# Kernel tuning notes

Measured on AMD Instinct MI355X. Metric: run time of the kernel, lower is better.

## Reference

```python
import jax, jax.numpy as jnp
import numpy as np


def setup_inputs() -> dict:
    key = jax.random.key(0)
    x = jax.random.normal(key, (16384, 4096), dtype=jnp.float32)
    return {"x": x, "k": 64}


def reference(x, k):
    # allow_negative_topk=False -> select and output based on ReLU(x)
    scores = jax.nn.relu(x)                      # [N, D]
    kk = min(k, scores.shape[-1])
    _, topk_idx = jax.lax.top_k(scores, kk)      # [N, kk]
    rows = jnp.arange(scores.shape[0])[:, None]  # [N, 1]
    mask = jnp.zeros_like(scores).at[rows, topk_idx].set(1.0)
    return scores * mask
```

## Files before the change

### kernel.cpp

```cpp
#include <hip/hip_runtime.h>


constexpr int ROW_LEN = 4096;
constexpr int TPB     = 256;
constexpr int SEG     = 128;
constexpr unsigned int KPRE_BITS = 0x3FC00000u;

typedef float f32x4 __attribute__((ext_vector_type(4)));

__global__ __launch_bounds__(TPB, 4)
void topk_relu_kernel(const float* __restrict__ x, const int* __restrict__ kptr,
                      float* __restrict__ out, int rows)
{
    __shared__ alignas(16) int hist[256];
    __shared__ unsigned int cand[4 * SEG];
    __shared__ int scnt[4];
    __shared__ unsigned int selT;
    __shared__ int selNeed;
    __shared__ int wtot[4];
    __shared__ unsigned long long wtot64[4];
    __shared__ int sel_digit, sel_kk, sel_flag;

    const int row = blockIdx.x;
    if (row >= rows) return;
    const int tid  = threadIdx.x;
    const int lane = tid & 63;
    const int wid  = tid >> 6;

    int k = *kptr;
    if (k > ROW_LEN) k = ROW_LEN;

    const float* __restrict__ xrow = x + (size_t)row * ROW_LEN;
    unsigned int key[16];
#pragma unroll
    for (int j = 0; j < 4; ++j) {
        f32x4 v = *(const f32x4*)(xrow + j * 1024 + tid * 4);
#pragma unroll
        for (int c = 0; c < 4; ++c)
            key[4 * j + c] = __float_as_uint(fmaxf(v[c], 0.0f));
    }

    int base = 0;
#pragma unroll
    for (int j = 0; j < 16; ++j) {
        const bool p = key[j] > KPRE_BITS;
        const unsigned long long mask = __ballot(p);
        const int prior = __builtin_amdgcn_mbcnt_hi(
            (unsigned int)(mask >> 32),
            __builtin_amdgcn_mbcnt_lo((unsigned int)mask, 0));
        const int idx = base + prior;
        if (p && idx < SEG) cand[(wid << 7) + idx] = key[j];
        base += (int)__popcll(mask);
    }
    if (lane == 0) scnt[wid] = base;
    __syncthreads();

    const int c0 = scnt[0], c1 = scnt[1], c2 = scnt[2], c3 = scnt[3];
    const int cnt = c0 + c1 + c2 + c3;
    const bool segok = (c0 <= SEG) & (c1 <= SEG) & (c2 <= SEG) & (c3 <= SEG);

    unsigned int T;
    int need;

    if (cnt >= k && segok) {
        if (wid == 0) {
            const int sc[4] = {c0, c1, c2, c3};
            unsigned int c[8];
#pragma unroll
            for (int i = 0; i < 8; ++i) {
                const int s   = i >> 1;
                const int off = lane + 64 * (i & 1);
                c[i] = (off < sc[s]) ? cand[(s << 7) + off] : 0u;
            }
            int kk = k;
            unsigned int prefix = 0;
#pragma unroll
            for (int p = 0; p < 4; ++p) {
                const int shift = 24 - 8 * p;
                ((int4*)hist)[lane] = make_int4(0, 0, 0, 0);
#pragma unroll
                for (int i = 0; i < 8; ++i) {
                    const unsigned int ci = c[i];
                    if (ci != 0u && (p == 0 || (ci >> (shift + 8)) == prefix))
                        atomicAdd(&hist[(ci >> shift) & 255u], 1);
                }
                const int4 h = ((const int4*)hist)[lane];
                const int h0 = h.x, h1 = h.y, h2 = h.z, h3 = h.w;
                const int lsum = h0 + h1 + h2 + h3;
                int suf = lsum;
#pragma unroll
                for (int d = 1; d < 64; d <<= 1) {
                    int v = __shfl_down(suf, d);
                    if (lane < 64 - d) suf += v;
                }
                const unsigned long long mm = __ballot(suf >= kk);
                const int L = 63 - __clzll(mm);
                int dig = 0, kkn = 0;
                if (lane == L) {
                    int cum = suf - lsum;
                    const int hh[4] = {h0, h1, h2, h3};
#pragma unroll
                    for (int b = 3; b >= 0; --b) {
                        if (cum + hh[b] >= kk) { dig = lane * 4 + b; kkn = kk - cum; break; }
                        cum += hh[b];
                    }
                }
                dig = __shfl(dig, L);
                kk  = __shfl(kkn, L);
                prefix = (prefix << 8) | (unsigned int)dig;
            }
            if (lane == 0) { selT = prefix; selNeed = kk; }
        }

        __syncthreads();
        T = selT;
        need = selNeed;
    } else {
        int kk = k;
        unsigned int prefix = 0;
        int t0 = 0;
        for (int p = 0; p < 4; ++p) {
            const int shift = 24 - 8 * p;
            hist[tid & 255] = 0;
            if (tid == 0) sel_flag = 0;
            __syncthreads();
#pragma unroll
            for (int j = 0; j < 16; ++j) {
                const unsigned int kj = key[j];
                if (kj != 0u && (p == 0 || (kj >> (shift + 8)) == prefix))
                    atomicAdd(&hist[(kj >> shift) & 255u], 1);
            }
            __syncthreads();
            if (tid < 64) {
                const int b0 = tid * 4;
                const int h0 = hist[b0 + 0], h1 = hist[b0 + 1];
                const int h2 = hist[b0 + 2], h3 = hist[b0 + 3];
                const int lsum = h0 + h1 + h2 + h3;
                int suf = lsum;
#pragma unroll
                for (int d = 1; d < 64; d <<= 1) {
                    int v = __shfl_down(suf, d);
                    if (lane < 64 - d) suf += v;
                }
                const unsigned long long mm = __ballot(suf >= kk);
                if (mm == 0ull) {
                    if (lane == 0) sel_flag = 1;
                } else {
                    const int L = 63 - __clzll(mm);
                    if (lane == L) {
                        int cum = suf - lsum;
                        const int hh[4] = {h0, h1, h2, h3};
#pragma unroll
                        for (int b = 3; b >= 0; --b) {
                            if (cum + hh[b] >= kk) { sel_digit = b0 + b; sel_kk = kk - cum; break; }
                            cum += hh[b];
                        }
                    }
                }
            }
            __syncthreads();
            if (sel_flag) { t0 = 1; break; }
            prefix = (prefix << 8) | (unsigned int)sel_digit;
            kk = sel_kk;
            __syncthreads();
        }
        if (t0) { T = 0u; need = 0; }
        else    { T = prefix; need = kk; }
    }

    int eqc = 0;
#pragma unroll
    for (int j = 0; j < 16; ++j) eqc += (key[j] == T) ? 1 : 0;
    int wsum = eqc;
#pragma unroll
    for (int d = 1; d < 64; d <<= 1) wsum += __shfl_down(wsum, d);
    if (lane == 0) wtot[wid] = wsum;
    __syncthreads();
    const int tot = wtot[0] + wtot[1] + wtot[2] + wtot[3];

    float* __restrict__ orow = out + (size_t)row * ROW_LEN;

    if (tot == need) {
#pragma unroll
        for (int j = 0; j < 4; ++j) {
            f32x4 v;
#pragma unroll
            for (int c2 = 0; c2 < 4; ++c2) {
                const unsigned int kj = key[4 * j + c2];
                v[c2] = (kj >= T && T != 0u) ? __uint_as_float(kj) : 0.0f;
            }
            *(f32x4*)(orow + j * 1024 + tid * 4) = v;
        }
    } else {
        unsigned long long packed = 0ull;
#pragma unroll
        for (int j = 0; j < 4; ++j) {
            int e = 0;
#pragma unroll
            for (int c = 0; c < 4; ++c) e += (key[4 * j + c] == T) ? 1 : 0;
            packed |= (unsigned long long)e << (16 * j);
        }
        unsigned long long incp = packed;
#pragma unroll
        for (int d = 1; d < 64; d <<= 1) {
            unsigned long long v = __shfl_up(incp, d);
            if (lane >= d) incp += v;
        }
        if (lane == 63) wtot64[wid] = incp;
        __syncthreads();
        unsigned long long b64 = 0ull;
        for (int w = 0; w < wid; ++w) b64 += wtot64[w];
        const unsigned long long exclp = b64 + incp - packed;
        const unsigned long long t64 = wtot64[0] + wtot64[1] + wtot64[2] + wtot64[3];
        int S[4];
        S[0] = 0;
        S[1] = (int)(t64 & 0xFFFFull);
        S[2] = S[1] + (int)((t64 >> 16) & 0xFFFFull);
        S[3] = S[2] + (int)((t64 >> 32) & 0xFFFFull);
#pragma unroll
        for (int j = 0; j < 4; ++j) {
            int rr = S[j] + (int)((exclp >> (16 * j)) & 0xFFFFull);
            f32x4 v;
#pragma unroll
            for (int c2 = 0; c2 < 4; ++c2) {
                const unsigned int kj = key[4 * j + c2];
                const bool eq = (kj == T);
                const bool keep = (kj > T) || (eq && rr < need);
                v[c2] = keep ? __uint_as_float(kj) : 0.0f;
                rr += eq ? 1 : 0;
            }
            *(f32x4*)(orow + j * 1024 + tid * 4) = v;
        }
    }
}

extern "C" void kernel_launch(void* const* d_in, const int* in_sizes, int n_in,
                              void* d_out, int out_size, void* d_ws, size_t ws_size,
                              hipStream_t stream)
{
    const float* x    = (const float*)d_in[0];
    const int*   kptr = (const int*)d_in[1];
    float*       out  = (float*)d_out;
    const int rows = in_sizes[0] / ROW_LEN;
    topk_relu_kernel<<<rows, TPB, 0, stream>>>(x, kptr, out, rows);
}
```

Baseline: 100.1 us.

## Process one row per wavefront instead of one row per block

```diff
diff --git a/kernel.cpp b/kernel.cpp
--- a/kernel.cpp
+++ b/kernel.cpp
@@ -3,7 +3,7 @@
 
 constexpr int ROW_LEN = 4096;
 constexpr int TPB     = 256;
-constexpr int SEG     = 128;
+constexpr int CAP     = 512;
 constexpr unsigned int KPRE_BITS = 0x3FC00000u;
 
 typedef float f32x4 __attribute__((ext_vector_type(4)));
@@ -12,88 +12,120 @@
 void topk_relu_kernel(const float* __restrict__ x, const int* __restrict__ kptr,
                       float* __restrict__ out, int rows)
 {
-    __shared__ alignas(16) int hist[256];
-    __shared__ unsigned int cand[4 * SEG];
-    __shared__ int scnt[4];
-    __shared__ unsigned int selT;
-    __shared__ int selNeed;
-    __shared__ int wtot[4];
-    __shared__ unsigned long long wtot64[4];
-    __shared__ int sel_digit, sel_kk, sel_flag;
-
-    const int row = blockIdx.x;
-    if (row >= rows) return;
+    __shared__ unsigned int cand4[4][CAP];
+    __shared__ alignas(16) int hist4[4][256];
+
     const int tid  = threadIdx.x;
     const int lane = tid & 63;
     const int wid  = tid >> 6;
 
+    const int row = blockIdx.x * 4 + wid;
+    if (row >= rows) return;
+
     int k = *kptr;
     if (k > ROW_LEN) k = ROW_LEN;
 
     const float* __restrict__ xrow = x + (size_t)row * ROW_LEN;
-    unsigned int key[16];
-#pragma unroll
-    for (int j = 0; j < 4; ++j) {
-        f32x4 v = *(const f32x4*)(xrow + j * 1024 + tid * 4);
+    unsigned int key[64];
+#pragma unroll
+    for (int j = 0; j < 16; ++j) {
+        f32x4 v = *(const f32x4*)(xrow + j * 256 + lane * 4);
 #pragma unroll
         for (int c = 0; c < 4; ++c)
             key[4 * j + c] = __float_as_uint(fmaxf(v[c], 0.0f));
     }
 
-    int base = 0;
-#pragma unroll
-    for (int j = 0; j < 16; ++j) {
+    unsigned int* __restrict__ cand = &cand4[wid][0];
+    int* __restrict__ hist = &hist4[wid][0];
+
+    int cnt = 0;
+#pragma unroll
+    for (int j = 0; j < 64; ++j) {
         const bool p = key[j] > KPRE_BITS;
         const unsigned long long mask = __ballot(p);
         const int prior = __builtin_amdgcn_mbcnt_hi(
             (unsigned int)(mask >> 32),
             __builtin_amdgcn_mbcnt_lo((unsigned int)mask, 0));
-        const int idx = base + prior;
-        if (p && idx < SEG) cand[(wid << 7) + idx] = key[j];
-        base += (int)__popcll(mask);
-    }
-    if (lane == 0) scnt[wid] = base;
-    __syncthreads();
-
-    const int c0 = scnt[0], c1 = scnt[1], c2 = scnt[2], c3 = scnt[3];
-    const int cnt = c0 + c1 + c2 + c3;
-    const bool segok = (c0 <= SEG) & (c1 <= SEG) & (c2 <= SEG) & (c3 <= SEG);
+        const int idx = cnt + prior;
+        if (p && idx < CAP) cand[idx] = key[j];
+        cnt += (int)__popcll(mask);
+    }
 
     unsigned int T;
     int need;
 
-    if (cnt >= k && segok) {
-        if (wid == 0) {
-            const int sc[4] = {c0, c1, c2, c3};
-            unsigned int c[8];
+    if (cnt >= k && cnt <= CAP) {
+        unsigned int c[8];
+#pragma unroll
+        for (int i = 0; i < 8; ++i) {
+            const int off = lane + 64 * i;
+            c[i] = (off < cnt) ? cand[off] : 0u;
+        }
+        int kk = k;
+        unsigned int prefix = 0;
+#pragma unroll
+        for (int p = 0; p < 4; ++p) {
+            const int shift = 24 - 8 * p;
+            ((int4*)hist)[lane] = make_int4(0, 0, 0, 0);
 #pragma unroll
             for (int i = 0; i < 8; ++i) {
-                const int s   = i >> 1;
-                const int off = lane + 64 * (i & 1);
-                c[i] = (off < sc[s]) ? cand[(s << 7) + off] : 0u;
-            }
-            int kk = k;
-            unsigned int prefix = 0;
-#pragma unroll
-            for (int p = 0; p < 4; ++p) {
-                const int shift = 24 - 8 * p;
-                ((int4*)hist)[lane] = make_int4(0, 0, 0, 0);
-#pragma unroll
-                for (int i = 0; i < 8; ++i) {
-                    const unsigned int ci = c[i];
-                    if (ci != 0u && (p == 0 || (ci >> (shift + 8)) == prefix))
-                        atomicAdd(&hist[(ci >> shift) & 255u], 1);
+                const unsigned int ci = c[i];
+                if (ci != 0u && (p == 0 || (ci >> (shift + 8)) == prefix))
+                    atomicAdd(&hist[(ci >> shift) & 255u], 1);
+            }
+            const int4 h = ((const int4*)hist)[lane];
+            const int h0 = h.x, h1 = h.y, h2 = h.z, h3 = h.w;
+            const int lsum = h0 + h1 + h2 + h3;
+            int suf = lsum;
+#pragma unroll
+            for (int d = 1; d < 64; d <<= 1) {
+                int v = __shfl_down(suf, d);
+                if (lane < 64 - d) suf += v;
+            }
+            const unsigned long long mm = __ballot(suf >= kk);
+            const int L = 63 - __clzll(mm);
+            int dig = 0, kkn = 0;
+            if (lane == L) {
+                int cum = suf - lsum;
+                const int hh[4] = {h0, h1, h2, h3};
+#pragma unroll
+                for (int b = 3; b >= 0; --b) {
+                    if (cum + hh[b] >= kk) { dig = lane * 4 + b; kkn = kk - cum; break; }
+                    cum += hh[b];
                 }
-                const int4 h = ((const int4*)hist)[lane];
-                const int h0 = h.x, h1 = h.y, h2 = h.z, h3 = h.w;
-                const int lsum = h0 + h1 + h2 + h3;
-                int suf = lsum;
-#pragma unroll
-                for (int d = 1; d < 64; d <<= 1) {
-                    int v = __shfl_down(suf, d);
-                    if (lane < 64 - d) suf += v;
-                }
-                const unsigned long long mm = __ballot(suf >= kk);
+            }
+            dig = __shfl(dig, L);
+            kk  = __shfl(kkn, L);
+            prefix = (prefix << 8) | (unsigned int)dig;
+        }
+        T = prefix;
+        need = kk;
+    } else {
+        int kk = k;
+        unsigned int prefix = 0;
+        bool t0 = false;
+        for (int p = 0; p < 4 && !t0; ++p) {
+            const int shift = 24 - 8 * p;
+            ((int4*)hist)[lane] = make_int4(0, 0, 0, 0);
+#pragma unroll
+            for (int j = 0; j < 64; ++j) {
+                const unsigned int kj = key[j];
+                if (kj != 0u && (p == 0 || (kj >> (shift + 8)) == prefix))
+                    atomicAdd(&hist[(kj >> shift) & 255u], 1);
+            }
+            const int4 h = ((const int4*)hist)[lane];
+            const int h0 = h.x, h1 = h.y, h2 = h.z, h3 = h.w;
+            const int lsum = h0 + h1 + h2 + h3;
+            int suf = lsum;
+#pragma unroll
+            for (int d = 1; d < 64; d <<= 1) {
+                int v = __shfl_down(suf, d);
+                if (lane < 64 - d) suf += v;
+            }
+            const unsigned long long mm = __ballot(suf >= kk);
+            if (mm == 0ull) {
+                t0 = true;
+            } else {
                 const int L = 63 - __clzll(mm);
                 int dig = 0, kkn = 0;
                 if (lane == L) {
@@ -109,60 +141,6 @@
                 kk  = __shfl(kkn, L);
                 prefix = (prefix << 8) | (unsigned int)dig;
             }
-            if (lane == 0) { selT = prefix; selNeed = kk; }
-        }
-
-        __syncthreads();
-        T = selT;
-        need = selNeed;
-    } else {
-        int kk = k;
-        unsigned int prefix = 0;
-        int t0 = 0;
-        for (int p = 0; p < 4; ++p) {
-            const int shift = 24 - 8 * p;
-            hist[tid & 255] = 0;
-            if (tid == 0) sel_flag = 0;
-            __syncthreads();
-#pragma unroll
-            for (int j = 0; j < 16; ++j) {
-                const unsigned int kj = key[j];
-                if (kj != 0u && (p == 0 || (kj >> (shift + 8)) == prefix))
-                    atomicAdd(&hist[(kj >> shift) & 255u], 1);
-            }
-            __syncthreads();
-            if (tid < 64) {
-                const int b0 = tid * 4;
-                const int h0 = hist[b0 + 0], h1 = hist[b0 + 1];
-                const int h2 = hist[b0 + 2], h3 = hist[b0 + 3];
-                const int lsum = h0 + h1 + h2 + h3;
-                int suf = lsum;
-#pragma unroll
-                for (int d = 1; d < 64; d <<= 1) {
-                    int v = __shfl_down(suf, d);
-                    if (lane < 64 - d) suf += v;
-                }
-                const unsigned long long mm = __ballot(suf >= kk);
-                if (mm == 0ull) {
-                    if (lane == 0) sel_flag = 1;
-                } else {
-                    const int L = 63 - __clzll(mm);
-                    if (lane == L) {
-                        int cum = suf - lsum;
-                        const int hh[4] = {h0, h1, h2, h3};
-#pragma unroll
-                        for (int b = 3; b >= 0; --b) {
-                            if (cum + hh[b] >= kk) { sel_digit = b0 + b; sel_kk = kk - cum; break; }
-                            cum += hh[b];
-                        }
-                    }
-                }
-            }
-            __syncthreads();
-            if (sel_flag) { t0 = 1; break; }
-            prefix = (prefix << 8) | (unsigned int)sel_digit;
-            kk = sel_kk;
-            __syncthreads();
         }
         if (t0) { T = 0u; need = 0; }
         else    { T = prefix; need = kk; }
@@ -170,56 +148,59 @@
 
     int eqc = 0;
 #pragma unroll
-    for (int j = 0; j < 16; ++j) eqc += (key[j] == T) ? 1 : 0;
-    int wsum = eqc;
-#pragma unroll
-    for (int d = 1; d < 64; d <<= 1) wsum += __shfl_down(wsum, d);
-    if (lane == 0) wtot[wid] = wsum;
-    __syncthreads();
-    const int tot = wtot[0] + wtot[1] + wtot[2] + wtot[3];
+    for (int j = 0; j < 64; ++j) eqc += (key[j] == T) ? 1 : 0;
+    int tot = eqc;
+#pragma unroll
+    for (int d = 1; d < 64; d <<= 1) tot += __shfl_xor(tot, d);
 
     float* __restrict__ orow = out + (size_t)row * ROW_LEN;
 
     if (tot == need) {
 #pragma unroll
-        for (int j = 0; j < 4; ++j) {
+        for (int j = 0; j < 16; ++j) {
             f32x4 v;
 #pragma unroll
             for (int c2 = 0; c2 < 4; ++c2) {
                 const unsigned int kj = key[4 * j + c2];
                 v[c2] = (kj >= T && T != 0u) ? __uint_as_float(kj) : 0.0f;
             }
-            *(f32x4*)(orow + j * 1024 + tid * 4) = v;
+            *(f32x4*)(orow + j * 256 + lane * 4) = v;
         }
     } else {
-        unsigned long long packed = 0ull;
-#pragma unroll
-        for (int j = 0; j < 4; ++j) {
-            int e = 0;
-#pragma unroll
-            for (int c = 0; c < 4; ++c) e += (key[4 * j + c] == T) ? 1 : 0;
-            packed |= (unsigned long long)e << (16 * j);
-        }
-        unsigned long long incp = packed;
-#pragma unroll
-        for (int d = 1; d < 64; d <<= 1) {
-            unsigned long long v = __shfl_up(incp, d);
-            if (lane >= d) incp += v;
-        }
-        if (lane == 63) wtot64[wid] = incp;
-        __syncthreads();
-        unsigned long long b64 = 0ull;
-        for (int w = 0; w < wid; ++w) b64 += wtot64[w];
-        const unsigned long long exclp = b64 + incp - packed;
-        const unsigned long long t64 = wtot64[0] + wtot64[1] + wtot64[2] + wtot64[3];
-        int S[4];
+        unsigned long long exclp[4];
+        int totj[16];
+#pragma unroll
+        for (int q = 0; q < 4; ++q) {
+            unsigned long long pk = 0ull;
+#pragma unroll
+            for (int jj = 0; jj < 4; ++jj) {
+                const int j = 4 * q + jj;
+                int e = 0;
+#pragma unroll
+                for (int c = 0; c < 4; ++c) e += (key[4 * j + c] == T) ? 1 : 0;
+                pk |= (unsigned long long)e << (16 * jj);
+            }
+            unsigned long long incp = pk;
+#pragma unroll
+            for (int d = 1; d < 64; d <<= 1) {
+                unsigned long long v = __shfl_up(incp, d);
+                if (lane >= d) incp += v;
+            }
+            exclp[q] = incp - pk;
+            const unsigned long long t = __shfl(incp, 63);
+#pragma unroll
+            for (int jj = 0; jj < 4; ++jj)
+                totj[4 * q + jj] = (int)((t >> (16 * jj)) & 0xFFFFull);
+        }
+        int S[16];
         S[0] = 0;
-        S[1] = (int)(t64 & 0xFFFFull);
-        S[2] = S[1] + (int)((t64 >> 16) & 0xFFFFull);
-        S[3] = S[2] + (int)((t64 >> 32) & 0xFFFFull);
-#pragma unroll
-        for (int j = 0; j < 4; ++j) {
-            int rr = S[j] + (int)((exclp >> (16 * j)) & 0xFFFFull);
+#pragma unroll
+        for (int j = 1; j < 16; ++j) S[j] = S[j - 1] + totj[j - 1];
+
+#pragma unroll
+        for (int j = 0; j < 16; ++j) {
+            const int q = j >> 2, jj = j & 3;
+            int rr = S[j] + (int)((exclp[q] >> (16 * jj)) & 0xFFFFull);
             f32x4 v;
 #pragma unroll
             for (int c2 = 0; c2 < 4; ++c2) {
@@ -229,7 +210,7 @@
                 v[c2] = keep ? __uint_as_float(kj) : 0.0f;
                 rr += eq ? 1 : 0;
             }
-            *(f32x4*)(orow + j * 1024 + tid * 4) = v;
+            *(f32x4*)(orow + j * 256 + lane * 4) = v;
         }
     }
 }
@@ -242,5 +223,6 @@
     const int*   kptr = (const int*)d_in[1];
     float*       out  = (float*)d_out;
     const int rows = in_sizes[0] / ROW_LEN;
-    topk_relu_kernel<<<rows, TPB, 0, stream>>>(x, kptr, out, rows);
+    const int nb = (rows + 3) / 4;
+    topk_relu_kernel<<<nb, TPB, 0, stream>>>(x, kptr, out, rows);
 }
```

Result: slower. 114.4 us (+14.4%).
